# Kernel tuning notes

Measured on AMD Instinct MI355X. Metric: run time of the kernel, lower is better.

The kernel has to match this reference:

```python
import jax, jax.numpy as jnp
import numpy as np

B, T, C = 256, 16384, 8


def setup_inputs() -> dict:
    key = jax.random.key(0)
    k1, k2, k3, k4, k5 = jax.random.split(key, 5)
    return {
        "emissions": jax.random.normal(k1, (B, T, C), dtype=jnp.float32),
        "tags": jax.random.randint(k2, (B, T), 0, C, dtype=jnp.int64),
        "mask": jnp.ones((B, T), dtype=bool),
        "transitions": jax.random.normal(k3, (C, C), dtype=jnp.float32) * 0.1,
        "start_transitions": jax.random.normal(k4, (C,), dtype=jnp.float32) * 0.1,
        "end_transitions": jax.random.normal(k5, (C,), dtype=jnp.float32) * 0.1,
    }


def _forward_alg(emissions, mask, transitions, start_transitions, end_transitions):
    # alpha: (B, C) log-partition recurrence over time
    alpha0 = start_transitions[None, :] + emissions[:, 0]

    def step(alpha, inputs):
        emit_t, mask_t = inputs  # (B, C), (B,)
        # (B, C_prev, C_next) semiring (logsumexp, +) step
        scores = alpha[:, :, None] + transitions[None, :, :] + emit_t[:, None, :]
        alpha_next = jax.nn.logsumexp(scores, axis=1)
        alpha = jnp.where(mask_t[:, None], alpha_next, alpha)
        return alpha, None

    emits = jnp.swapaxes(emissions[:, 1:], 0, 1)  # (T-1, B, C)
    masks = jnp.swapaxes(mask[:, 1:], 0, 1)       # (T-1, B)
    alpha, _ = jax.lax.scan(step, alpha0, (emits, masks))
    alpha = alpha + end_transitions[None, :]
    return jax.nn.logsumexp(alpha, axis=1)  # (B,)


def reference(emissions, tags, mask, transitions, start_transitions, end_transitions):
    mask = mask.astype(bool)
    maskf = mask.astype(emissions.dtype)

    # Gold path score, fully vectorized over T
    emit_scores = jnp.take_along_axis(emissions, tags[:, :, None], axis=2)[:, :, 0]  # (B, T)
    trans_scores = transitions[tags[:, :-1], tags[:, 1:]]  # (B, T-1)
    score = start_transitions[tags[:, 0]] + emit_scores[:, 0]
    score = score + jnp.sum((emit_scores[:, 1:] + trans_scores) * maskf[:, 1:], axis=1)

    last_valid = jnp.sum(mask.astype(jnp.int32), axis=1) - 1  # (B,)
    last_tags = jnp.take_along_axis(tags, last_valid[:, None].astype(tags.dtype), axis=1)[:, 0]
    score = score + end_transitions[last_tags]

    log_Z = _forward_alg(emissions, mask, transitions, start_transitions, end_transitions)
    return -(score - log_Z)  # (B,) negative log-likelihood
```

## Files before the change

kernel.cpp:

```cpp
#include <hip/hip_runtime.h>


typedef float v2f __attribute__((ext_vector_type(2)));

#define Bn 256
#define Tn 16384
#define Kc 256
#define LOG2E 1.44269504088896340736f
#define LN2f  0.693147180559945309417f

static __device__ __forceinline__ v2f splat2(float x){ v2f r; r.x=x; r.y=x; return r; }
static __device__ __forceinline__ float ex2(float x){ return __builtin_amdgcn_exp2f(x); }
static __device__ __forceinline__ float lg2(float x){ return __builtin_amdgcn_logf(x); }

template<int CTRL>
static __device__ __forceinline__ int qdppi(int x){
    return __builtin_amdgcn_mov_dpp(x, CTRL, 0xf, 0xf, true);
}
template<int CTRL>
static __device__ __forceinline__ float qdppf(float x){
    return __int_as_float(qdppi<CTRL>(__float_as_int(x)));
}
template<int CTRL>
static __device__ __forceinline__ v2f qdppv(v2f x){
    v2f r; r.x = qdppf<CTRL>(x.x); r.y = qdppf<CTRL>(x.y); return r;
}
static __device__ __forceinline__ float qmax4(float x){
    x = fmaxf(x, qdppf<0xB1>(x));
    x = fmaxf(x, qdppf<0x4E>(x));
    return x;
}
static __device__ __forceinline__ float qsum4(float x){
    x += qdppf<0xB1>(x);
    x += qdppf<0x4E>(x);
    return x;
}

#define Q0(x) qdppi<0x00>(x)
#define Q1(x) qdppi<0x55>(x)
#define Q2(x) qdppi<0xAA>(x)
#define Q3(x) qdppi<0xFF>(x)

__global__ __launch_bounds__(256, 4)
void crf_chunks(const float* __restrict__ em, const int* __restrict__ tags,
                const float* __restrict__ trans, const float* __restrict__ start_t,
                float* __restrict__ part, float* __restrict__ dir)
{
    __shared__ float trans_s[64];
    __shared__ __align__(16) char stageb[4 * 4352];

    const int tid = threadIdx.x;
    if (tid < 64) trans_s[tid] = trans[tid];

    const int w   = tid >> 6;
    const int ln  = tid & 63;
    const int q   = ln >> 2;
    const int l   = ln & 3;
    const int blk = blockIdx.x;
    const int b   = blk >> 2;
    const int wave_c0 = ((blk & 3) << 6) | (w << 4);
    const int c   = wave_c0 | q;
    const int bc  = c << 6;
    const bool isz = (c == 0);

    const float* erow = em   + (size_t)b * Tn * 8;
    const int*   trow = tags + (size_t)b * Tn;

    const int sreg = ln >> 4;
    const int spos = ln & 15;
    const int base0 = (((wave_c0 + sreg) << 6) - 7) + (spos >> 1);
    const int hoff  = (ln & 1) << 2;

#define GLOAD(P_, T_, D_) do { \
    int t_ = base0 + ((P_) << 8) + ((T_) << 3); \
    t_ = (t_ < 0) ? 0 : t_; t_ = (t_ > Tn - 1) ? Tn - 1 : t_; \
    D_ = *(const float4*)(erow + ((size_t)t_ << 3) + hoff); } while(0)

    char* swave = stageb + w * 4352;
    char* swr   = swave + sreg * 272 + spos * 16;
#define SWRITE(P_, S_) *(float4*)(swr + (P_) * 1088) = (S_)

    const char* rb  = swave + q * 272 + l * 8;
    const char* rb2 = swave + q * 272;

    v2f E0,E1,E2r,E3,E4,E5,E6,E7;
    {
        const v2f* tp2 = (const v2f*)trans;
        #define MKE(K_, D_) { v2f t_ = tp2[(K_)*4 + l]; D_.x = ex2(t_.x*LOG2E); D_.y = ex2(t_.y*LOG2E); }
        MKE(0,E0) MKE(1,E1) MKE(2,E2r) MKE(3,E3) MKE(4,E4) MKE(5,E5) MKE(6,E6) MKE(7,E7)
        #undef MKE
    }
    const v2f sp = *(const v2f*)(start_t + 2 * l);

    int4 qt0, qt1, qt2, qt3;
    {
        const int4* tp = (const int4*)(trow + bc + (l << 4));
        qt0 = tp[0]; qt1 = tp[1]; qt2 = tp[2]; qt3 = tp[3];
    }
    const int t64 = trow[min(bc + 64, Tn - 1)];

    float4 gA0, gA1, gA2, gA3, gB0, gB1, gB2, gB3;
#define GLA(T_) do { GLOAD(0,T_,gA0); GLOAD(1,T_,gA1); GLOAD(2,T_,gA2); GLOAD(3,T_,gA3); } while(0)
#define GLB(T_) do { GLOAD(0,T_,gB0); GLOAD(1,T_,gB1); GLOAD(2,T_,gB2); GLOAD(3,T_,gB3); } while(0)
#define SWA do { SWRITE(0,gA0); SWRITE(1,gA1); SWRITE(2,gA2); SWRITE(3,gA3); } while(0)
#define SWB do { SWRITE(0,gB0); SWRITE(1,gB1); SWRITE(2,gB2); SWRITE(3,gB3); } while(0)

    GLA(0); GLB(1);
    SWA;
    GLA(2);
    __syncthreads();

    v2f v = splat2(1.f);
    int   etot = 0;
    float lam = 0.f, spart = 0.f;

#define MATVEC(A_) do { \
    v2f b0_ = qdppv<0x00>(v), b1_ = qdppv<0x55>(v), b2_ = qdppv<0xAA>(v), b3_ = qdppv<0xFF>(v); \
    A_ = splat2(b0_.x) * E0; \
    A_ = __builtin_elementwise_fma(splat2(b0_.y), E1,  A_); \
    A_ = __builtin_elementwise_fma(splat2(b1_.x), E2r, A_); \
    A_ = __builtin_elementwise_fma(splat2(b1_.y), E3,  A_); \
    A_ = __builtin_elementwise_fma(splat2(b2_.x), E4,  A_); \
    A_ = __builtin_elementwise_fma(splat2(b2_.y), E5,  A_); \
    A_ = __builtin_elementwise_fma(splat2(b3_.x), E6,  A_); \
    A_ = __builtin_elementwise_fma(splat2(b3_.y), E7,  A_); } while(0)

#define RENORM do { \
    float m_ = qmax4(fmaxf(v.x, v.y)); \
    int e_ = (__float_as_int(m_) >> 23) - 127; \
    float sc_ = __int_as_float((127 - e_) << 23); \
    etot += e_; \
    v *= splat2(sc_); } while(0)

#define WSTEP(U_) do { \
    v2f e2_ = *(const v2f*)(rb + (U_) * 32); \
    v2f w2_; w2_.x = ex2(e2_.x * LOG2E); w2_.y = ex2(e2_.y * LOG2E); \
    v2f a_; MATVEC(a_); \
    if (!isz) v = a_ * w2_; } while(0)

    WSTEP(0); WSTEP(1); WSTEP(2); WSTEP(3); WSTEP(4); WSTEP(5); WSTEP(6);

    {
        v2f e2_ = *(const v2f*)(rb + 7 * 32);
        v2f w2_; w2_.x = ex2(e2_.x * LOG2E); w2_.y = ex2(e2_.y * LOG2E);
        v2f a_; MATVEC(a_);
        if (isz) {
            v.x = ex2((e2_.x + sp.x) * LOG2E);
            v.y = ex2((e2_.y + sp.y) * LOG2E);
            etot = 0;
        } else v = a_ * w2_;
        RENORM;
        float s8_ = qsum4(v.x + v.y);
        lam = isz ? 0.f : (lg2(s8_) + (float)etot) * LN2f;
    }

    int prevt = Q0(qt0.x);

#define GSTEP(U_, CEXPR_) do { \
    v2f e2_ = *(const v2f*)(rb + ((U_) & 7) * 32); \
    v2f w2_; w2_.x = ex2(e2_.x * LOG2E); w2_.y = ex2(e2_.y * LOG2E); \
    v2f a_; MATVEC(a_); \
    const int cv_ = (CEXPR_); \
    const float emv_ = *(const float*)(rb2 + ((U_) & 7) * 32 + (cv_ << 2)); \
    if ((U_) != 71 || (bc + 64) < Tn) {       \
        v = a_ * w2_; \
        spart += emv_ + trans_s[(prevt << 3) + cv_]; \
    } \
    prevt = cv_; \
    if (((U_) & 7) == 7) RENORM; } while(0)


    SWB; GLB(3);
    GSTEP(8,  Q0(qt0.y)); GSTEP(9,  Q0(qt0.z)); GSTEP(10, Q0(qt0.w)); GSTEP(11, Q0(qt1.x));
    GSTEP(12, Q0(qt1.y)); GSTEP(13, Q0(qt1.z)); GSTEP(14, Q0(qt1.w)); GSTEP(15, Q0(qt2.x));

    SWA; GLA(4);
    GSTEP(16, Q0(qt2.y)); GSTEP(17, Q0(qt2.z)); GSTEP(18, Q0(qt2.w)); GSTEP(19, Q0(qt3.x));
    GSTEP(20, Q0(qt3.y)); GSTEP(21, Q0(qt3.z)); GSTEP(22, Q0(qt3.w)); GSTEP(23, Q1(qt0.x));

    SWB; GLB(5);
    GSTEP(24, Q1(qt0.y)); GSTEP(25, Q1(qt0.z)); GSTEP(26, Q1(qt0.w)); GSTEP(27, Q1(qt1.x));
    GSTEP(28, Q1(qt1.y)); GSTEP(29, Q1(qt1.z)); GSTEP(30, Q1(qt1.w)); GSTEP(31, Q1(qt2.x));

    SWA; GLA(6);
    GSTEP(32, Q1(qt2.y)); GSTEP(33, Q1(qt2.z)); GSTEP(34, Q1(qt2.w)); GSTEP(35, Q1(qt3.x));
    GSTEP(36, Q1(qt3.y)); GSTEP(37, Q1(qt3.z)); GSTEP(38, Q1(qt3.w)); GSTEP(39, Q2(qt0.x));

    SWB; GLB(7);
    GSTEP(40, Q2(qt0.y)); GSTEP(41, Q2(qt0.z)); GSTEP(42, Q2(qt0.w)); GSTEP(43, Q2(qt1.x));
    GSTEP(44, Q2(qt1.y)); GSTEP(45, Q2(qt1.z)); GSTEP(46, Q2(qt1.w)); GSTEP(47, Q2(qt2.x));

    SWA; GLA(8);
    GSTEP(48, Q2(qt2.y)); GSTEP(49, Q2(qt2.z)); GSTEP(50, Q2(qt2.w)); GSTEP(51, Q2(qt3.x));
    GSTEP(52, Q2(qt3.y)); GSTEP(53, Q2(qt3.z)); GSTEP(54, Q2(qt3.w)); GSTEP(55, Q3(qt0.x));

    SWB;
    GSTEP(56, Q3(qt0.y)); GSTEP(57, Q3(qt0.z)); GSTEP(58, Q3(qt0.w)); GSTEP(59, Q3(qt1.x));
    GSTEP(60, Q3(qt1.y)); GSTEP(61, Q3(qt1.z)); GSTEP(62, Q3(qt1.w)); GSTEP(63, Q3(qt2.x));

    SWA;
    GSTEP(64, Q3(qt2.y)); GSTEP(65, Q3(qt2.z)); GSTEP(66, Q3(qt2.w)); GSTEP(67, Q3(qt3.x));
    GSTEP(68, Q3(qt3.y)); GSTEP(69, Q3(qt3.z)); GSTEP(70, Q3(qt3.w)); GSTEP(71, t64);

    float sv_  = qsum4(v.x + v.y);
    float lamp = (lg2(sv_) + (float)etot) * LN2f;

    if (l == 0) part[(size_t)b * Kc + c] = (lamp - lam) - spart;

    if (c == Kc - 1) {
        dir[b * 8 + 2 * l]     = (lg2(v.x) + (float)etot) * LN2f - lamp;
        dir[b * 8 + 2 * l + 1] = (lg2(v.y) + (float)etot) * LN2f - lamp;
    }
}

__global__ __launch_bounds__(64)
void crf_combine(const float* __restrict__ em, const int* __restrict__ tags,
                 const float* __restrict__ start_t, const float* __restrict__ end_t,
                 const float* __restrict__ part, const float* __restrict__ dir,
                 float* __restrict__ out)
{
    const int b = blockIdx.x;
    const int lane = threadIdx.x;
    const float4 pv = *(const float4*)(part + (size_t)b * Kc + (lane << 2));
    float s = (pv.x + pv.y) + (pv.z + pv.w);
    #pragma unroll
    for (int m = 32; m >= 1; m >>= 1) s += __shfl_xor(s, m);

    const int j = lane & 7;
    float y = dir[b*8 + j] + end_t[j];
    float mx = y;
    mx = fmaxf(mx, __shfl_xor(mx, 1));
    mx = fmaxf(mx, __shfl_xor(mx, 2));
    mx = fmaxf(mx, __shfl_xor(mx, 4));
    float p = ex2((y - mx) * LOG2E);
    p += __shfl_xor(p, 1); p += __shfl_xor(p, 2); p += __shfl_xor(p, 4);
    float lse = mx + lg2(p) * LN2f;

    if (lane == 0) {
        int tg0 = tags[(size_t)b*Tn];
        int tgl = tags[(size_t)b*Tn + Tn - 1];
        float s0 = start_t[tg0] + em[(size_t)b*Tn*8 + tg0];
        float se = end_t[tgl];
        out[b] = s + lse - s0 - se;
    }
}

extern "C" void kernel_launch(void* const* d_in, const int* in_sizes, int n_in,
                              void* d_out, int out_size, void* d_ws, size_t ws_size,
                              hipStream_t stream) {
    const float* emissions   = (const float*)d_in[0];
    const int*   tags        = (const int*)d_in[1];
    const float* transitions = (const float*)d_in[3];
    const float* start_t     = (const float*)d_in[4];
    const float* end_t       = (const float*)d_in[5];
    float* out = (float*)d_out;

    float* part = (float*)d_ws;
    float* dir  = (float*)((char*)d_ws + (size_t)Bn*Kc*4);

    crf_chunks<<<dim3(Bn * 4), dim3(256), 0, stream>>>(
        emissions, tags, transitions, start_t, part, dir);
    crf_combine<<<dim3(Bn), dim3(64), 0, stream>>>(
        emissions, tags, start_t, end_t, part, dir, out);
}
```

Baseline: 217.0 us.

## Move gold-path score computation from chunk kernel into combine kernel

Removes the tag loads, DPP tag broadcasts, LDS emission gathers and transition lookups from the latency-bound chunked forward recurrence, along with the shared transition table and the block barrier it needed. The combine kernel now uses 256 threads per batch row to gather gold-path emission and transition scores per 64-step chunk, then reduces them together with the partition partials. This shortens the serial inner loop of the main kernel. In exchange, the second kernel becomes heavier, with scattered emission reads and an LDS reduction running after the main kernel.

```diff
diff --git a/kernel.cpp b/kernel.cpp
--- a/kernel.cpp
+++ b/kernel.cpp
@@ -36,22 +36,14 @@
     return x;
 }
 
-#define Q0(x) qdppi<0x00>(x)
-#define Q1(x) qdppi<0x55>(x)
-#define Q2(x) qdppi<0xAA>(x)
-#define Q3(x) qdppi<0xFF>(x)
-
 __global__ __launch_bounds__(256, 4)
-void crf_chunks(const float* __restrict__ em, const int* __restrict__ tags,
-                const float* __restrict__ trans, const float* __restrict__ start_t,
+void crf_chunks(const float* __restrict__ em, const float* __restrict__ trans,
+                const float* __restrict__ start_t,
                 float* __restrict__ part, float* __restrict__ dir)
 {
-    __shared__ float trans_s[64];
     __shared__ __align__(16) char stageb[4 * 4352];
 
     const int tid = threadIdx.x;
-    if (tid < 64) trans_s[tid] = trans[tid];
-
     const int w   = tid >> 6;
     const int ln  = tid & 63;
     const int q   = ln >> 2;
@@ -63,8 +55,7 @@
     const int bc  = c << 6;
     const bool isz = (c == 0);
 
-    const float* erow = em   + (size_t)b * Tn * 8;
-    const int*   trow = tags + (size_t)b * Tn;
+    const float* erow = em + (size_t)b * Tn * 8;
 
     const int sreg = ln >> 4;
     const int spos = ln & 15;
@@ -80,8 +71,7 @@
     char* swr   = swave + sreg * 272 + spos * 16;
 #define SWRITE(P_, S_) *(float4*)(swr + (P_) * 1088) = (S_)
 
-    const char* rb  = swave + q * 272 + l * 8;
-    const char* rb2 = swave + q * 272;
+    const char* rb = swave + q * 272 + l * 8;
 
     v2f E0,E1,E2r,E3,E4,E5,E6,E7;
     {
@@ -92,13 +82,6 @@
     }
     const v2f sp = *(const v2f*)(start_t + 2 * l);
 
-    int4 qt0, qt1, qt2, qt3;
-    {
-        const int4* tp = (const int4*)(trow + bc + (l << 4));
-        qt0 = tp[0]; qt1 = tp[1]; qt2 = tp[2]; qt3 = tp[3];
-    }
-    const int t64 = trow[min(bc + 64, Tn - 1)];
-
     float4 gA0, gA1, gA2, gA3, gB0, gB1, gB2, gB3;
 #define GLA(T_) do { GLOAD(0,T_,gA0); GLOAD(1,T_,gA1); GLOAD(2,T_,gA2); GLOAD(3,T_,gA3); } while(0)
 #define GLB(T_) do { GLOAD(0,T_,gB0); GLOAD(1,T_,gB1); GLOAD(2,T_,gB2); GLOAD(3,T_,gB3); } while(0)
@@ -108,11 +91,10 @@
     GLA(0); GLB(1);
     SWA;
     GLA(2);
-    __syncthreads();
 
     v2f v = splat2(1.f);
     int   etot = 0;
-    float lam = 0.f, spart = 0.f;
+    float lam = 0.f;
 
 #define MATVEC(A_) do { \
     v2f b0_ = qdppv<0x00>(v), b1_ = qdppv<0x55>(v), b2_ = qdppv<0xAA>(v), b3_ = qdppv<0xFF>(v); \
@@ -154,58 +136,30 @@
         lam = isz ? 0.f : (lg2(s8_) + (float)etot) * LN2f;
     }
 
-    int prevt = Q0(qt0.x);
-
-#define GSTEP(U_, CEXPR_) do { \
+#define GSTEP(U_) do { \
     v2f e2_ = *(const v2f*)(rb + ((U_) & 7) * 32); \
     v2f w2_; w2_.x = ex2(e2_.x * LOG2E); w2_.y = ex2(e2_.y * LOG2E); \
     v2f a_; MATVEC(a_); \
-    const int cv_ = (CEXPR_); \
-    const float emv_ = *(const float*)(rb2 + ((U_) & 7) * 32 + (cv_ << 2)); \
-    if ((U_) != 71 || (bc + 64) < Tn) {       \
+    if ((U_) != 71 || (bc + 64) < Tn)         \
         v = a_ * w2_; \
-        spart += emv_ + trans_s[(prevt << 3) + cv_]; \
-    } \
-    prevt = cv_; \
     if (((U_) & 7) == 7) RENORM; } while(0)
 
-
-    SWB; GLB(3);
-    GSTEP(8,  Q0(qt0.y)); GSTEP(9,  Q0(qt0.z)); GSTEP(10, Q0(qt0.w)); GSTEP(11, Q0(qt1.x));
-    GSTEP(12, Q0(qt1.y)); GSTEP(13, Q0(qt1.z)); GSTEP(14, Q0(qt1.w)); GSTEP(15, Q0(qt2.x));
-
-    SWA; GLA(4);
-    GSTEP(16, Q0(qt2.y)); GSTEP(17, Q0(qt2.z)); GSTEP(18, Q0(qt2.w)); GSTEP(19, Q0(qt3.x));
-    GSTEP(20, Q0(qt3.y)); GSTEP(21, Q0(qt3.z)); GSTEP(22, Q0(qt3.w)); GSTEP(23, Q1(qt0.x));
-
-    SWB; GLB(5);
-    GSTEP(24, Q1(qt0.y)); GSTEP(25, Q1(qt0.z)); GSTEP(26, Q1(qt0.w)); GSTEP(27, Q1(qt1.x));
-    GSTEP(28, Q1(qt1.y)); GSTEP(29, Q1(qt1.z)); GSTEP(30, Q1(qt1.w)); GSTEP(31, Q1(qt2.x));
-
-    SWA; GLA(6);
-    GSTEP(32, Q1(qt2.y)); GSTEP(33, Q1(qt2.z)); GSTEP(34, Q1(qt2.w)); GSTEP(35, Q1(qt3.x));
-    GSTEP(36, Q1(qt3.y)); GSTEP(37, Q1(qt3.z)); GSTEP(38, Q1(qt3.w)); GSTEP(39, Q2(qt0.x));
-
-    SWB; GLB(7);
-    GSTEP(40, Q2(qt0.y)); GSTEP(41, Q2(qt0.z)); GSTEP(42, Q2(qt0.w)); GSTEP(43, Q2(qt1.x));
-    GSTEP(44, Q2(qt1.y)); GSTEP(45, Q2(qt1.z)); GSTEP(46, Q2(qt1.w)); GSTEP(47, Q2(qt2.x));
-
-    SWA; GLA(8);
-    GSTEP(48, Q2(qt2.y)); GSTEP(49, Q2(qt2.z)); GSTEP(50, Q2(qt2.w)); GSTEP(51, Q2(qt3.x));
-    GSTEP(52, Q2(qt3.y)); GSTEP(53, Q2(qt3.z)); GSTEP(54, Q2(qt3.w)); GSTEP(55, Q3(qt0.x));
-
-    SWB;
-    GSTEP(56, Q3(qt0.y)); GSTEP(57, Q3(qt0.z)); GSTEP(58, Q3(qt0.w)); GSTEP(59, Q3(qt1.x));
-    GSTEP(60, Q3(qt1.y)); GSTEP(61, Q3(qt1.z)); GSTEP(62, Q3(qt1.w)); GSTEP(63, Q3(qt2.x));
-
-    SWA;
-    GSTEP(64, Q3(qt2.y)); GSTEP(65, Q3(qt2.z)); GSTEP(66, Q3(qt2.w)); GSTEP(67, Q3(qt3.x));
-    GSTEP(68, Q3(qt3.y)); GSTEP(69, Q3(qt3.z)); GSTEP(70, Q3(qt3.w)); GSTEP(71, t64);
+#define GS8(U0_) GSTEP(U0_); GSTEP(U0_+1); GSTEP(U0_+2); GSTEP(U0_+3); \
+                 GSTEP(U0_+4); GSTEP(U0_+5); GSTEP(U0_+6); GSTEP(U0_+7)
+
+    SWB; GLB(3);  GS8(8);
+    SWA; GLA(4);  GS8(16);
+    SWB; GLB(5);  GS8(24);
+    SWA; GLA(6);  GS8(32);
+    SWB; GLB(7);  GS8(40);
+    SWA; GLA(8);  GS8(48);
+    SWB;          GS8(56);
+    SWA;          GS8(64);
 
     float sv_  = qsum4(v.x + v.y);
     float lamp = (lg2(sv_) + (float)etot) * LN2f;
 
-    if (l == 0) part[(size_t)b * Kc + c] = (lamp - lam) - spart;
+    if (l == 0) part[(size_t)b * Kc + c] = lamp - lam;
 
     if (c == Kc - 1) {
         dir[b * 8 + 2 * l]     = (lg2(v.x) + (float)etot) * LN2f - lamp;
@@ -213,35 +167,79 @@
     }
 }
 
-__global__ __launch_bounds__(64)
+__global__ __launch_bounds__(256)
 void crf_combine(const float* __restrict__ em, const int* __restrict__ tags,
+                 const float* __restrict__ trans,
                  const float* __restrict__ start_t, const float* __restrict__ end_t,
                  const float* __restrict__ part, const float* __restrict__ dir,
                  float* __restrict__ out)
 {
+    __shared__ float trans_l[64];
+    __shared__ float red[256];
     const int b = blockIdx.x;
-    const int lane = threadIdx.x;
-    const float4 pv = *(const float4*)(part + (size_t)b * Kc + (lane << 2));
-    float s = (pv.x + pv.y) + (pv.z + pv.w);
-    #pragma unroll
-    for (int m = 32; m >= 1; m >>= 1) s += __shfl_xor(s, m);
-
-    const int j = lane & 7;
-    float y = dir[b*8 + j] + end_t[j];
-    float mx = y;
-    mx = fmaxf(mx, __shfl_xor(mx, 1));
-    mx = fmaxf(mx, __shfl_xor(mx, 2));
-    mx = fmaxf(mx, __shfl_xor(mx, 4));
-    float p = ex2((y - mx) * LOG2E);
-    p += __shfl_xor(p, 1); p += __shfl_xor(p, 2); p += __shfl_xor(p, 4);
-    float lse = mx + lg2(p) * LN2f;
-
-    if (lane == 0) {
-        int tg0 = tags[(size_t)b*Tn];
-        int tgl = tags[(size_t)b*Tn + Tn - 1];
-        float s0 = start_t[tg0] + em[(size_t)b*Tn*8 + tg0];
-        float se = end_t[tgl];
-        out[b] = s + lse - s0 - se;
+    const int c = threadIdx.x;
+    if (c < 64) trans_l[c] = trans[c];
+    __syncthreads();
+
+    const float* erow = em   + (size_t)b * Tn * 8;
+    const int*   trow = tags + (size_t)b * Tn;
+
+    int4 x0,x1,x2,x3,x4,x5,x6,x7,x8,x9,x10,x11,x12,x13,x14,x15;
+    {
+        const int4* tp = (const int4*)(trow + (c << 6));
+        x0=tp[0]; x1=tp[1]; x2=tp[2]; x3=tp[3]; x4=tp[4]; x5=tp[5]; x6=tp[6]; x7=tp[7];
+        x8=tp[8]; x9=tp[9]; x10=tp[10]; x11=tp[11]; x12=tp[12]; x13=tp[13]; x14=tp[14]; x15=tp[15];
+    }
+    const int t64v = trow[min((c << 6) + 64, Tn - 1)];
+
+    float sp_ = 0.f;
+    int   pv_ = x0.x;
+#define GG(T_, CV_) do { const int cv_ = (CV_); \
+    sp_ += erow[((size_t)((c << 6) + (T_)) << 3) + cv_] + trans_l[(pv_ << 3) + cv_]; \
+    pv_ = cv_; } while(0)
+
+    GG(1,x0.y);  GG(2,x0.z);  GG(3,x0.w);  GG(4,x1.x);  GG(5,x1.y);  GG(6,x1.z);  GG(7,x1.w);
+    GG(8,x2.x);  GG(9,x2.y);  GG(10,x2.z); GG(11,x2.w); GG(12,x3.x); GG(13,x3.y); GG(14,x3.z);
+    GG(15,x3.w); GG(16,x4.x); GG(17,x4.y); GG(18,x4.z); GG(19,x4.w); GG(20,x5.x); GG(21,x5.y);
+    GG(22,x5.z); GG(23,x5.w); GG(24,x6.x); GG(25,x6.y); GG(26,x6.z); GG(27,x6.w); GG(28,x7.x);
+    GG(29,x7.y); GG(30,x7.z); GG(31,x7.w); GG(32,x8.x); GG(33,x8.y); GG(34,x8.z); GG(35,x8.w);
+    GG(36,x9.x); GG(37,x9.y); GG(38,x9.z); GG(39,x9.w); GG(40,x10.x);GG(41,x10.y);GG(42,x10.z);
+    GG(43,x10.w);GG(44,x11.x);GG(45,x11.y);GG(46,x11.z);GG(47,x11.w);GG(48,x12.x);GG(49,x12.y);
+    GG(50,x12.z);GG(51,x12.w);GG(52,x13.x);GG(53,x13.y);GG(54,x13.z);GG(55,x13.w);GG(56,x14.x);
+    GG(57,x14.y);GG(58,x14.z);GG(59,x14.w);GG(60,x15.x);GG(61,x15.y);GG(62,x15.z);GG(63,x15.w);
+    if (c < 255) {
+        sp_ += erow[((size_t)((c << 6) + 64) << 3) + t64v] + trans_l[(pv_ << 3) + t64v];
+    }
+
+    red[c] = part[(size_t)b * Kc + c] - sp_;
+    __syncthreads();
+    if (c < 128) red[c] += red[c + 128];
+    __syncthreads();
+    if (c < 64)  red[c] += red[c + 64];
+    __syncthreads();
+
+    if (c < 64) {
+        float s = red[c];
+        #pragma unroll
+        for (int m = 32; m >= 1; m >>= 1) s += __shfl_xor(s, m);
+
+        const int j = c & 7;
+        float y = dir[b*8 + j] + end_t[j];
+        float mx = y;
+        mx = fmaxf(mx, __shfl_xor(mx, 1));
+        mx = fmaxf(mx, __shfl_xor(mx, 2));
+        mx = fmaxf(mx, __shfl_xor(mx, 4));
+        float p = ex2((y - mx) * LOG2E);
+        p += __shfl_xor(p, 1); p += __shfl_xor(p, 2); p += __shfl_xor(p, 4);
+        float lse = mx + lg2(p) * LN2f;
+
+        if (c == 0) {
+            const int tg0 = x0.x;
+            const int tgl = trow[Tn - 1];
+            float s0 = start_t[tg0] + erow[tg0];
+            float se = end_t[tgl];
+            out[b] = s + lse - s0 - se;
+        }
     }
 }
 
@@ -259,7 +257,7 @@
     float* dir  = (float*)((char*)d_ws + (size_t)Bn*Kc*4);
 
     crf_chunks<<<dim3(Bn * 4), dim3(256), 0, stream>>>(
-        emissions, tags, transitions, start_t, part, dir);
-    crf_combine<<<dim3(Bn), dim3(64), 0, stream>>>(
-        emissions, tags, start_t, end_t, part, dir, out);
-}
+        emissions, transitions, start_t, part, dir);
+    crf_combine<<<dim3(Bn), dim3(256), 0, stream>>>(
+        emissions, tags, transitions, start_t, end_t, part, dir, out);
+}
```

Measured after the change: 244.6 us. 12.7% more time.
